# Optimization experiments

Hardware: AMD Instinct MI355X
Metric: run time of the kernel (lower is better)

Reference implementation:

```python
import jax, jax.numpy as jnp
import numpy as np

N_NODES = 50000   # r_mat is [N_NODES, N_NODES] sparse
N_REL = 1000      # number of relations (rows of dual_layer)
D = 128           # node / relation feature dim
NNZ = 800000      # number of edges (nnz of r_mat)


def setup_inputs() -> dict:
    key = jax.random.key(0)
    k1, k2, k3, k4, k5, k6 = jax.random.split(key, 6)
    return {
        "inlayer": jax.random.normal(k1, (N_NODES, D), jnp.float32),
        "dual_layer": jax.random.normal(k2, (N_REL, D), jnp.float32),
        # Conv1d(in=D, out=1, kernel=1): weight [1, D, 1] -> vector [D], bias [1]
        "conv_w": jax.random.normal(k3, (D,), jnp.float32) * (1.0 / np.sqrt(D)),
        "conv_b": jax.random.normal(k4, (1,), jnp.float32) * 0.01,
        # COO indices of r_mat: row = destination node, col = source node
        "edge_idx": jax.random.randint(k5, (2, NNZ), 0, N_NODES, dtype=jnp.int32),
        # r_mat._values(): integer relation id per edge
        "edge_rel": jax.random.randint(k6, (NNZ,), 0, N_REL, dtype=jnp.int32),
    }


def reference(inlayer, dual_layer, conv_w, conv_b, edge_idx, edge_rel):
    # conv1d with kernel_size=1 over [1, D, n_rel] == per-relation linear -> [n_rel]
    scores = dual_layer @ conv_w + conv_b[0]
    # gather per-edge logit by relation id
    logits = scores[edge_rel]                                  # [nnz]
    # NOTE: original applies leaky_relu then softmax GLOBALLY over all nnz edges
    coefs = jax.nn.softmax(jax.nn.leaky_relu(logits))          # [nnz]
    row, col = edge_idx[0], edge_idx[1]
    # sparse-dense matmul: out[r] = sum_{e: row[e]=r} coefs[e] * inlayer[col[e]]
    out = jax.ops.segment_sum(coefs[:, None] * inlayer[col], row,
                              num_segments=N_NODES)            # [N, D]
    # act_func=None path of the original forward
    return out
```

## Files before the change

kernel.cpp:

```cpp
#include <hip/hip_runtime.h>
#include <hip/hip_fp16.h>
#include <math.h>

#define N_NODES 50000
#define N_REL   1000
#define D       128
#define NNZ     800000

#define RB    512
#define NBIN  98
#define CAP   10240
#define CH    2048
#define NCH   ((NNZ + CH - 1) / CH)
#define K1T   512
#define K1E   (CH / K1T)
#define SRB   64
#define CAPL  1536

__global__ void __launch_bounds__(512)
k0_kernel(const float* __restrict__ dual, const float* __restrict__ conv_w,
          const float* __restrict__ conv_b, float* __restrict__ exp_scores) {
    int wid = (blockIdx.x * 512 + threadIdx.x) >> 6;
    int lane = threadIdx.x & 63;
    if (wid >= N_REL) return;
    const float* row = dual + (long)wid * D;
    float s = row[lane] * conv_w[lane] + row[lane + 64] * conv_w[lane + 64];
    #pragma unroll
    for (int off = 32; off > 0; off >>= 1) s += __shfl_down(s, off);
    if (lane == 0) {
        float v = s + conv_b[0];
        v = (v >= 0.f) ? v : 0.01f * v;
        exp_scores[wid] = expf(v);
    }
}

__global__ void __launch_bounds__(K1T)
k1_kernel(const int* __restrict__ rows, const int* __restrict__ cols,
          const int* __restrict__ rel, const float* __restrict__ inlayer,
          const float* __restrict__ exp_scores, float* __restrict__ denom,
          unsigned* __restrict__ bincur, unsigned long long* __restrict__ binbuf,
          __half2* __restrict__ hinl) {
    __shared__ unsigned long long sbuf[CH];
    __shared__ unsigned char sbin[CH];
    __shared__ unsigned lcnt[NBIN], lstart[NBIN], lgb[NBIN];
    __shared__ float fpart[8];
    __shared__ unsigned w0sum;
    int t = threadIdx.x;
    int gtid = blockIdx.x * K1T + t;
    int lane = t & 63, w = t >> 6;

    const float4* src4 = (const float4*)inlayer;
    uint2* dst2 = (uint2*)hinl;
    for (int i = gtid; i < N_NODES * D / 4; i += NCH * K1T) {
        float4 f = src4[i];
        __half2 h0 = __floats2half2_rn(f.x, f.y);
        __half2 h1 = __floats2half2_rn(f.z, f.w);
        uint2 o; o.x = *(unsigned*)&h0; o.y = *(unsigned*)&h1;
        dst2[i] = o;
    }

    if (t < NBIN) lcnt[t] = 0;
    __syncthreads();

    int n = NNZ - blockIdx.x * CH; if (n > CH) n = CH;
    int base4 = blockIdx.x * (CH / 4);

    int       ebin[K1E];
    unsigned  erank[K1E];
    unsigned long long epack[K1E];
    float dsum = 0.f;
    bool has = (4 * t < n);
    int4 rr, cc, qq;
    if (has) {
        rr = ((const int4*)rows)[base4 + t];
        cc = ((const int4*)cols)[base4 + t];
        qq = ((const int4*)rel)[base4 + t];
    }
    #pragma unroll
    for (int k = 0; k < K1E; ++k) {
        if (has) {
            int r = (k == 0) ? rr.x : (k == 1) ? rr.y : (k == 2) ? rr.z : rr.w;
            int c = (k == 0) ? cc.x : (k == 1) ? cc.y : (k == 2) ? cc.z : cc.w;
            int q = (k == 0) ? qq.x : (k == 1) ? qq.y : (k == 2) ? qq.z : qq.w;
            int b = r >> 9;
            epack[k] = (unsigned long long)(unsigned)c
                     | ((unsigned long long)(unsigned)q << 16)
                     | ((unsigned long long)(unsigned)(r & 511) << 26);
            ebin[k] = b;
            erank[k] = atomicAdd(&lcnt[b], 1u);
            dsum += exp_scores[q];
        } else ebin[k] = -1;
    }
    #pragma unroll
    for (int off = 32; off > 0; off >>= 1) dsum += __shfl_down(dsum, off);
    if (lane == 0) fpart[w] = dsum;
    __syncthreads();

    unsigned v = (t < NBIN) ? lcnt[t] : 0u;
    if (t < 128) {
        #pragma unroll
        for (int off = 1; off < 64; off <<= 1) {
            unsigned y = __shfl_up(v, off);
            if (lane >= off) v += y;
        }
        if (t == 63) w0sum = v;
    }
    if (t == 0) {
        float s = 0.f;
        #pragma unroll
        for (int k = 0; k < 8; ++k) s += fpart[k];
        atomicAdd(denom, s);
    }
    __syncthreads();
    if (t >= 64 && t < 128) v += w0sum;
    if (t < NBIN) {
        lstart[t] = v - lcnt[t];
        lgb[t] = atomicAdd(&bincur[t * 16], lcnt[t]);
    }
    __syncthreads();

    #pragma unroll
    for (int k = 0; k < K1E; ++k) {
        if (ebin[k] >= 0) {
            unsigned p = lstart[ebin[k]] + erank[k];
            sbuf[p] = epack[k];
            sbin[p] = (unsigned char)ebin[k];
        }
    }
    __syncthreads();

    #pragma unroll
    for (int k = 0; k < K1E; ++k) {
        int j = k * K1T + t;
        if (j < n) {
            int b = sbin[j];
            unsigned slot = lgb[b] + (unsigned)j - lstart[b];
            if (slot < CAP)
                binbuf[(unsigned long long)b * CAP + slot] = sbuf[j];
        }
    }
}

__global__ void __launch_bounds__(512)
k2_kernel(const unsigned* __restrict__ bincur,
          const unsigned long long* __restrict__ binbuf,
          const float* __restrict__ exp_scores,
          const float* __restrict__ denom,
          const __half2* __restrict__ hinl, float* __restrict__ out) {
    __shared__ unsigned ulist[CAPL];
    __shared__ unsigned list[CAPL];
    __shared__ unsigned cnt[SRB], ex[SRB], cur[SRB];
    __shared__ unsigned total;
    int t = threadIdx.x, lane = t & 63, w = t >> 6;
    int b   = blockIdx.x >> 3;
    int sub = blockIdx.x & 7;

    if (t < SRB) cnt[t] = 0;
    if (t == 0) total = 0;
    float inv = 1.0f / *denom;

    __syncthreads();

    unsigned nb = bincur[b * 16]; if (nb > CAP) nb = CAP;
    const unsigned long long* bb = binbuf + (unsigned long long)b * CAP;

    for (unsigned e0 = 0; e0 < nb; e0 += 2048u) {
        unsigned i0 = e0 + (unsigned)t;
        unsigned long long p0 = 0, p1 = 0, p2 = 0, p3 = 0;
        bool g0 = i0 < nb, g1 = i0 + 512u < nb,
             g2 = i0 + 1024u < nb, g3 = i0 + 1536u < nb;
        if (g0) p0 = bb[i0];
        if (g1) p1 = bb[i0 + 512u];
        if (g2) p2 = bb[i0 + 1024u];
        if (g3) p3 = bb[i0 + 1536u];
        #define PROC(pk, g)                                                  \
        if (g) {                                                             \
            unsigned u_ = (unsigned)((pk) >> 26) & 511u;                     \
            if ((u_ >> 6) == (unsigned)sub) {                                \
                unsigned lo_ = (unsigned)(pk);                               \
                unsigned idx_ = atomicAdd(&total, 1u);                       \
                if (idx_ < CAPL) ulist[idx_] = lo_;                          \
                atomicAdd(&cnt[lo_ >> 26], 1u);                              \
            }                                                                \
        }
        PROC(p0, g0) PROC(p1, g1) PROC(p2, g2) PROC(p3, g3)
        #undef PROC
    }
    __syncthreads();

    if (t < 64) {
        unsigned c0 = cnt[t];
        unsigned v = c0;
        #pragma unroll
        for (int off = 1; off < 64; off <<= 1) {
            unsigned y = __shfl_up(v, off);
            if (lane >= off) v += y;
        }
        ex[t] = v - c0;
        cur[t] = v - c0;
    }
    __syncthreads();

    unsigned tot = total; if (tot > CAPL) tot = CAPL;
    for (unsigned i = t; i < tot; i += 512u) {
        unsigned lo = ulist[i];
        unsigned idx = atomicAdd(&cur[lo >> 26], 1u);
        if (idx < CAPL) list[idx] = lo & 0x3FFFFFFu;
    }
    __syncthreads();

    int quad = lane >> 4;
    int l16  = lane & 15;
    for (int i = 0; i < 8; ++i) {
        int rl = w * 8 + i;
        int node = b * RB + sub * SRB + rl;
        int s0 = (int)ex[rl];
        int e0 = s0 + (int)cnt[rl];
        if (e0 > CAPL) e0 = CAPL;
        float a0=0.f,a1=0.f,a2=0.f,a3=0.f,a4=0.f,a5=0.f,a6=0.f,a7=0.f;
        for (int base = s0; base < e0; base += 64) {
            int rem = e0 - base; if (rem > 64) rem = 64;
            int px = 0, py = 0;
            if (lane < rem) {
                unsigned pk = list[base + lane];
                px = (int)(pk & 0xFFFFu);
                py = __float_as_int(exp_scores[pk >> 16]);
            }
            for (int jj = 0; jj < rem; jj += 16) {
                #pragma unroll
                for (int k = 0; k < 16; k += 4) {
                    if (jj + k < rem) {
                        int idx = jj + k + quad;
                        int   c = __shfl(px, idx);
                        float wv = __int_as_float(__shfl(py, idx));
                        const __half2* hp = hinl + (long)c * (D / 2) + l16 * 4;
                        uint4 hv = *(const uint4*)hp;
                        float2 f0 = __half22float2(*(const __half2*)&hv.x);
                        float2 f1 = __half22float2(*(const __half2*)&hv.y);
                        float2 f2 = __half22float2(*(const __half2*)&hv.z);
                        float2 f3 = __half22float2(*(const __half2*)&hv.w);
                        a0 += wv * f0.x; a1 += wv * f0.y;
                        a2 += wv * f1.x; a3 += wv * f1.y;
                        a4 += wv * f2.x; a5 += wv * f2.y;
                        a6 += wv * f3.x; a7 += wv * f3.y;
                    }
                }
            }
        }
        #define COMB(x) x += __shfl(x, lane ^ 16); x += __shfl(x, lane ^ 32);
        COMB(a0) COMB(a1) COMB(a2) COMB(a3) COMB(a4) COMB(a5) COMB(a6) COMB(a7)
        #undef COMB
        if (lane < 32 && node < N_NODES) {
            float4 o;
            int hi = (lane >> 4) & 1;
            if (hi) { o.x = a4*inv; o.y = a5*inv; o.z = a6*inv; o.w = a7*inv; }
            else    { o.x = a0*inv; o.y = a1*inv; o.z = a2*inv; o.w = a3*inv; }
            *(float4*)(out + (long)node * D + l16 * 8 + hi * 4) = o;
        }
    }
}

extern "C" void kernel_launch(void* const* d_in, const int* in_sizes, int n_in,
                              void* d_out, int out_size, void* d_ws, size_t ws_size,
                              hipStream_t stream) {
    const float* inlayer  = (const float*)d_in[0];
    const float* dual     = (const float*)d_in[1];
    const float* conv_w   = (const float*)d_in[2];
    const float* conv_b   = (const float*)d_in[3];
    const int*   edge_idx = (const int*)d_in[4];
    const int*   edge_rel = (const int*)d_in[5];
    float* out = (float*)d_out;
    const int* rows = edge_idx;
    const int* cols = edge_idx + NNZ;

    char* ws = (char*)d_ws;
    float*              exp_scores = (float*)             (ws);
    float*              denom      = (float*)             (ws + 4096);
    unsigned*           bincur     = (unsigned*)          (ws + 8192);
    unsigned long long* binbuf     = (unsigned long long*)(ws + 16384);
    __half2*            hinl       = (__half2*)           (ws + 16384 + 8028160);

    hipMemsetAsync(ws + 4096, 0, 12288, stream);

    k0_kernel<<<125, 512, 0, stream>>>(dual, conv_w, conv_b, exp_scores);
    k1_kernel<<<NCH, K1T, 0, stream>>>(rows, cols, edge_rel, inlayer, exp_scores,
                                       denom, bincur, binbuf, hinl);
    k2_kernel<<<NBIN * 8, 512, 0, stream>>>(bincur, binbuf, exp_scores, denom,
                                            hinl, out);
}
```

Baseline: 139.9 us.

## Add second-level binning pass so each sub-block reads only its own edges

Before, each of the 8 sub-blocks per bin scanned the whole bin (up to 10240 64-bit entries) and kept only its eighth, so every bin was read eight times. A new k2a kernel splits each bin into 8 sub-bins of 32-bit packed entries, using a local counting sort and global atomic offsets. The gather kernel then reads only its own sub-bin. This costs an extra kernel launch and one extra write and read of the edge list. It also adds a per-sub-bin capacity limit (SCAP) that could truncate edges if a sub-bin overflows.

```diff
diff --git a/kernel.cpp b/kernel.cpp
--- a/kernel.cpp
+++ b/kernel.cpp
@@ -14,8 +14,11 @@
 #define NCH   ((NNZ + CH - 1) / CH)
 #define K1T   512
 #define K1E   (CH / K1T)
+#define QW    2560
+#define QE    (QW / 512)
 #define SRB   64
-#define CAPL  1536
+#define SCAP  1536
+#define NSUB  (NBIN * 8)
 
 __global__ void __launch_bounds__(512)
 k0_kernel(const float* __restrict__ dual, const float* __restrict__ conv_w,
@@ -142,49 +145,91 @@
 }
 
 __global__ void __launch_bounds__(512)
-k2_kernel(const unsigned* __restrict__ bincur,
-          const unsigned long long* __restrict__ binbuf,
-          const float* __restrict__ exp_scores,
-          const float* __restrict__ denom,
+k2a_kernel(const unsigned* __restrict__ bincur,
+           const unsigned long long* __restrict__ binbuf,
+           unsigned* __restrict__ scur, unsigned* __restrict__ subbuf) {
+    __shared__ unsigned sbuf[QW];
+    __shared__ unsigned char ssl[QW];
+    __shared__ unsigned lcnt[8], lstart[8], lgb[8];
+    int t = threadIdx.x;
+    int b = blockIdx.x >> 2;
+    int q = blockIdx.x & 3;
+    unsigned nb = bincur[b * 16]; if (nb > CAP) nb = CAP;
+    int lo = q * QW;
+    int n = (int)nb - lo; if (n > QW) n = QW; if (n < 0) n = 0;
+
+    if (t < 8) lcnt[t] = 0;
+    __syncthreads();
+
+    unsigned pk32[QE]; int esl[QE]; unsigned erank[QE];
+    #pragma unroll
+    for (int k = 0; k < QE; ++k) {
+        int j = k * 512 + t;
+        if (j < n) {
+            unsigned long long pk = binbuf[(unsigned long long)b * CAP + lo + j];
+            unsigned u = (unsigned)(pk >> 26) & 511u;
+            int s = (int)(u >> 6);
+            pk32[k] = ((unsigned)pk & 0x3FFFFFFu) | ((u & 63u) << 26);
+            esl[k] = s;
+            erank[k] = atomicAdd(&lcnt[s], 1u);
+        } else esl[k] = -1;
+    }
+    __syncthreads();
+
+    if (t < 8) lgb[t] = atomicAdd(&scur[(b * 8 + t) * 16], lcnt[t]);
+    if (t == 0) {
+        unsigned acc = 0;
+        #pragma unroll
+        for (int s = 0; s < 8; ++s) { lstart[s] = acc; acc += lcnt[s]; }
+    }
+    __syncthreads();
+
+    #pragma unroll
+    for (int k = 0; k < QE; ++k) {
+        if (esl[k] >= 0) {
+            unsigned p = lstart[esl[k]] + erank[k];
+            sbuf[p] = pk32[k];
+            ssl[p] = (unsigned char)esl[k];
+        }
+    }
+    __syncthreads();
+
+    #pragma unroll
+    for (int k = 0; k < QE; ++k) {
+        int j = k * 512 + t;
+        if (j < n) {
+            int s = ssl[j];
+            unsigned slot = lgb[s] + (unsigned)j - lstart[s];
+            if (slot < SCAP)
+                subbuf[(unsigned)(b * 8 + s) * SCAP + slot] = sbuf[j];
+        }
+    }
+}
+
+__global__ void __launch_bounds__(512)
+k3_kernel(const unsigned* __restrict__ scur, const unsigned* __restrict__ subbuf,
+          const float* __restrict__ exp_scores, const float* __restrict__ denom,
           const __half2* __restrict__ hinl, float* __restrict__ out) {
-    __shared__ unsigned ulist[CAPL];
-    __shared__ unsigned list[CAPL];
+    __shared__ unsigned list[SCAP];
     __shared__ unsigned cnt[SRB], ex[SRB], cur[SRB];
-    __shared__ unsigned total;
     int t = threadIdx.x, lane = t & 63, w = t >> 6;
-    int b   = blockIdx.x >> 3;
-    int sub = blockIdx.x & 7;
+    int sid = blockIdx.x;
+    int b = sid >> 3, sub = sid & 7;
+    unsigned n = scur[sid * 16]; if (n > SCAP) n = SCAP;
+    const unsigned* sb = subbuf + (unsigned)sid * SCAP;
 
     if (t < SRB) cnt[t] = 0;
-    if (t == 0) total = 0;
     float inv = 1.0f / *denom;
-
-    __syncthreads();
-
-    unsigned nb = bincur[b * 16]; if (nb > CAP) nb = CAP;
-    const unsigned long long* bb = binbuf + (unsigned long long)b * CAP;
-
-    for (unsigned e0 = 0; e0 < nb; e0 += 2048u) {
-        unsigned i0 = e0 + (unsigned)t;
-        unsigned long long p0 = 0, p1 = 0, p2 = 0, p3 = 0;
-        bool g0 = i0 < nb, g1 = i0 + 512u < nb,
-             g2 = i0 + 1024u < nb, g3 = i0 + 1536u < nb;
-        if (g0) p0 = bb[i0];
-        if (g1) p1 = bb[i0 + 512u];
-        if (g2) p2 = bb[i0 + 1024u];
-        if (g3) p3 = bb[i0 + 1536u];
-        #define PROC(pk, g)                                                  \
-        if (g) {                                                             \
-            unsigned u_ = (unsigned)((pk) >> 26) & 511u;                     \
-            if ((u_ >> 6) == (unsigned)sub) {                                \
-                unsigned lo_ = (unsigned)(pk);                               \
-                unsigned idx_ = atomicAdd(&total, 1u);                       \
-                if (idx_ < CAPL) ulist[idx_] = lo_;                          \
-                atomicAdd(&cnt[lo_ >> 26], 1u);                              \
-            }                                                                \
-        }
-        PROC(p0, g0) PROC(p1, g1) PROC(p2, g2) PROC(p3, g3)
-        #undef PROC
+    __syncthreads();
+
+    unsigned pkr[3];
+    #pragma unroll
+    for (int k = 0; k < 3; ++k) {
+        int e = k * 512 + t;
+        if (e < (int)n) {
+            pkr[k] = sb[e];
+            atomicAdd(&cnt[pkr[k] >> 26], 1u);
+        }
     }
     __syncthreads();
 
@@ -201,11 +246,13 @@
     }
     __syncthreads();
 
-    unsigned tot = total; if (tot > CAPL) tot = CAPL;
-    for (unsigned i = t; i < tot; i += 512u) {
-        unsigned lo = ulist[i];
-        unsigned idx = atomicAdd(&cur[lo >> 26], 1u);
-        if (idx < CAPL) list[idx] = lo & 0x3FFFFFFu;
+    #pragma unroll
+    for (int k = 0; k < 3; ++k) {
+        int e = k * 512 + t;
+        if (e < (int)n) {
+            unsigned idx = atomicAdd(&cur[pkr[k] >> 26], 1u);
+            if (idx < SCAP) list[idx] = pkr[k] & 0x3FFFFFFu;
+        }
     }
     __syncthreads();
 
@@ -216,7 +263,7 @@
         int node = b * RB + sub * SRB + rl;
         int s0 = (int)ex[rl];
         int e0 = s0 + (int)cnt[rl];
-        if (e0 > CAPL) e0 = CAPL;
+        if (e0 > SCAP) e0 = SCAP;
         float a0=0.f,a1=0.f,a2=0.f,a3=0.f,a4=0.f,a5=0.f,a6=0.f,a7=0.f;
         for (int base = s0; base < e0; base += 64) {
             int rem = e0 - base; if (rem > 64) rem = 64;
@@ -277,14 +324,17 @@
     float*              exp_scores = (float*)             (ws);
     float*              denom      = (float*)             (ws + 4096);
     unsigned*           bincur     = (unsigned*)          (ws + 8192);
-    unsigned long long* binbuf     = (unsigned long long*)(ws + 16384);
-    __half2*            hinl       = (__half2*)           (ws + 16384 + 8028160);
-
-    hipMemsetAsync(ws + 4096, 0, 12288, stream);
+    unsigned*           scur       = (unsigned*)          (ws + 16384);
+    unsigned long long* binbuf     = (unsigned long long*)(ws + 69632);
+    unsigned*           subbuf     = (unsigned*)          (ws + 69632 + 8028160);
+    __half2*            hinl       = (__half2*)           (ws + 69632 + 8028160 + 4816896);
+
+    hipMemsetAsync(ws + 4096, 0, 65536 - 4096 + 784 * 64 - (65536 - 16384), stream);
 
     k0_kernel<<<125, 512, 0, stream>>>(dual, conv_w, conv_b, exp_scores);
     k1_kernel<<<NCH, K1T, 0, stream>>>(rows, cols, edge_rel, inlayer, exp_scores,
                                        denom, bincur, binbuf, hinl);
-    k2_kernel<<<NBIN * 8, 512, 0, stream>>>(bincur, binbuf, exp_scores, denom,
-                                            hinl, out);
-}
+    k2a_kernel<<<NBIN * 4, 512, 0, stream>>>(bincur, binbuf, scur, subbuf);
+    k3_kernel<<<NSUB, 512, 0, stream>>>(scur, subbuf, exp_scores, denom,
+                                        hinl, out);
+}
```

Measured after the change: 138.0 us. Within noise of the previous version (-1.3%).
